# Optimization experiments

Measured on AMD Instinct MI355X. Metric: run time of the kernel, lower is better.

Reference implementation:

```python
import jax, jax.numpy as jnp
import numpy as np


def setup_inputs() -> dict:
    key = jax.random.key(0)
    kq, kk, kv = jax.random.split(key, 3)
    B, HQ, HKV, S, D = 1, 32, 8, 2048, 128
    return {
        "query": jax.random.normal(kq, (B, HQ, S, D), dtype=jnp.float32),
        "key": jax.random.normal(kk, (B, HKV, S, D), dtype=jnp.float32),
        "value": jax.random.normal(kv, (B, HKV, S, D), dtype=jnp.float32),
    }


def reference(query, key, value):
    # RawSDP.forward with is_causal=True, attn_mask=None, dropout_p=0, scale=None
    b, hq, sq, d = query.shape
    hkv = key.shape[1]
    reps = hq // hkv  # GQA group size
    # repeak_kv: expand each kv head `reps` times contiguously along head axis
    key = jnp.repeat(key, reps, axis=1)    # [b, hq, skv, d]
    value = jnp.repeat(value, reps, axis=1)
    skv = key.shape[2]
    half_sqrt = 1.0 / jnp.sqrt(jnp.sqrt(jnp.float32(d)))  # scale split across q and k
    scores = jnp.einsum("bhqd,bhkd->bhqk", query * half_sqrt, key * half_sqrt)
    # causal tril bool mask -> additive mask (0 where allowed, finfo.min where not)
    causal = jnp.tril(jnp.ones((sq, skv), dtype=bool))
    neg = jnp.finfo(query.dtype).min
    scores = scores + jnp.where(causal, jnp.zeros((), query.dtype), neg)
    # softmax computed in float32, cast back to query dtype
    attn = jax.nn.softmax(scores.astype(jnp.float32), axis=-1).astype(query.dtype)
    return jnp.einsum("bhqk,bhkd->bhqd", attn, value)
```

## Files before the change

### kernel.cpp

```cpp
#include <hip/hip_runtime.h>
#include <hip/hip_bf16.h>
#include <stdint.h>

typedef __attribute__((ext_vector_type(8))) short bf16x8;
typedef __attribute__((ext_vector_type(4))) float f32x4;
typedef __attribute__((ext_vector_type(16))) float f32x16;

#define S_LEN 2048
#define D_DIM 128
#define HQ_N  32
#define KVB   32
#define NT    64
#define KTILE_B 8192
#define VTILE_B 8192

__device__ __forceinline__ ushort f2bf(float f) {
  union { float f; uint32_t u; } c; c.f = f;
  uint32_t u = c.u;
  u += 0x7FFFu + ((u >> 16) & 1u);
  return (ushort)(u >> 16);
}

__device__ __forceinline__ uint32_t cvtpk(float lo, float hi) {
  uint32_t r;
  asm("v_cvt_pk_bf16_f32 %0, %1, %2" : "=v"(r) : "v"(lo), "v"(hi));
  return r;
}

__global__ __launch_bounds__(256) void prep_k(const float* __restrict__ K,
                                              ushort* __restrict__ KT) {
  int tid  = blockIdx.x * 256 + threadIdx.x;
  int tile = tid >> 9;
  int c    = tid & 511;
  int s    = c >> 6;
  int lane = c & 63;
  int l31  = lane & 31, hi = lane >> 5;
  const float* src = K + ((size_t)(tile * 32 + l31)) * D_DIM + 16 * s + 8 * hi;
  float4 x = *(const float4*)src;
  float4 y = *(const float4*)(src + 4);
  union { ushort u[8]; bf16x8 v; } o;
  o.u[0] = f2bf(x.x); o.u[1] = f2bf(x.y); o.u[2] = f2bf(x.z); o.u[3] = f2bf(x.w);
  o.u[4] = f2bf(y.x); o.u[5] = f2bf(y.y); o.u[6] = f2bf(y.z); o.u[7] = f2bf(y.w);
  *(bf16x8*)(KT + (size_t)tid * 8) = o.v;
}

__global__ __launch_bounds__(256) void prep_v(const float* __restrict__ V,
                                              ushort* __restrict__ VT) {
  int tid  = blockIdx.x * 256 + threadIdx.x;
  int tile = tid >> 9;
  int cc   = tid & 511;
  int l31  = cc & 31;
  int hi   = (cc >> 5) & 1;
  int c    = (cc >> 6) & 1;
  int dt   = cc >> 7;
  int hkv  = tile >> 6, kt = tile & 63;
  const float* src = V + ((size_t)hkv * S_LEN + kt * 32 + 16 * c + 8 * hi) * D_DIM
                       + 32 * dt + l31;
  union { ushort u[8]; bf16x8 v; } o;
  #pragma unroll
  for (int jj = 0; jj < 8; ++jj) o.u[jj] = f2bf(src[(size_t)jj * D_DIM]);
  *(bf16x8*)(VT + (size_t)tid * 8) = o.v;
}

__global__ __launch_bounds__(64, 2) void attn_fwd(
    const float* __restrict__ Q, const ushort* __restrict__ KT,
    const ushort* __restrict__ VT, float* __restrict__ O) {
  const int id   = blockIdx.x;
  const int g    = id & 7;
  const int rest = id >> 3;
  const int qh   = rest & 3;
  const int j    = 63 - (rest >> 2);
  const int h    = g * 4 + qh;
  const int lane = threadIdx.x;
  const int l31  = lane & 31;
  const int hi   = lane >> 5;
  const int qrow = j * 32 + l31;

  const char* kt_base = (const char*)KT + (size_t)g * NT * KTILE_B;
  const char* vt_base = (const char*)VT + (size_t)g * NT * VTILE_B;

  const float scale = 0.08838834764831845f * 1.4426950408889634f;
  bf16x8 qf[8];
  {
    const float* qp = Q + ((size_t)h * S_LEN + qrow) * D_DIM;
    #pragma unroll
    for (int s = 0; s < 8; ++s) {
      const float* p = qp + 16 * s + 8 * hi;
      float4 x = *(const float4*)p;
      float4 y = *(const float4*)(p + 4);
      bf16x8 f;
      f[0] = (short)f2bf(x.x * scale); f[1] = (short)f2bf(x.y * scale);
      f[2] = (short)f2bf(x.z * scale); f[3] = (short)f2bf(x.w * scale);
      f[4] = (short)f2bf(y.x * scale); f[5] = (short)f2bf(y.y * scale);
      f[6] = (short)f2bf(y.z * scale); f[7] = (short)f2bf(y.w * scale);
      qf[s] = f;
    }
  }

  f32x16 o4[4] = {};
  float mrow = -1e30f, lsum = 0.f;

  for (int kt = 0; kt <= j; ++kt) {
    const char* kp = kt_base + (size_t)kt * KTILE_B;
    const char* vp = vt_base + (size_t)kt * VTILE_B;

    bf16x8 kf[8], vf[8];
    #pragma unroll
    for (int s = 0; s < 8; ++s)
      kf[s] = *(const bf16x8*)(kp + (s * 64 + lane) * 16);
    #pragma unroll
    for (int u = 0; u < 8; ++u)
      vf[u] = *(const bf16x8*)(vp + (u * 64 + lane) * 16);

    f32x16 st = {};
    __builtin_amdgcn_s_setprio(1);
    #pragma unroll
    for (int s = 0; s < 8; ++s)
      st = __builtin_amdgcn_mfma_f32_32x32x16_bf16(kf[s], qf[s], st, 0, 0, 0);
    __builtin_amdgcn_s_setprio(0);

    if (kt == j) {
      #pragma unroll
      for (int r = 0; r < 16; ++r) {
        int kv = KVB * kt + (r & 3) + 8 * (r >> 2) + 4 * hi;
        if (kv > qrow) st[r] = -1e30f;
      }
    }

    float t8[8];
    #pragma unroll
    for (int e = 0; e < 8; ++e) t8[e] = fmaxf(st[e], st[e + 8]);
    float mx = fmaxf(fmaxf(fmaxf(t8[0], t8[1]), fmaxf(t8[2], t8[3])),
                     fmaxf(fmaxf(t8[4], t8[5]), fmaxf(t8[6], t8[7])));
    mx = fmaxf(mx, __shfl_xor(mx, 32));
    float mnew = fmaxf(mrow, mx);
    float alpha = exp2f(mrow - mnew);
    mrow = mnew;

    #pragma unroll
    for (int e = 0; e < 16; ++e) st[e] = exp2f(st[e] - mnew);
    float s8[8];
    #pragma unroll
    for (int e = 0; e < 8; ++e) s8[e] = st[e] + st[e + 8];
    float rsum = ((s8[0] + s8[1]) + (s8[2] + s8[3])) +
                 ((s8[4] + s8[5]) + (s8[6] + s8[7]));
    rsum += __shfl_xor(rsum, 32);
    lsum = lsum * alpha + rsum;

    #pragma unroll
    for (int dt = 0; dt < 4; ++dt) o4[dt] *= alpha;

    bf16x8 pb[2];
    #pragma unroll
    for (int c = 0; c < 2; ++c) {
      const int r0 = c * 8;
      uint32_t a0 = cvtpk(st[r0 + 0], st[r0 + 1]);
      uint32_t b0 = cvtpk(st[r0 + 4], st[r0 + 5]);
      asm volatile("v_permlane32_swap_b32 %0, %1" : "+v"(a0), "+v"(b0));
      uint32_t a1 = cvtpk(st[r0 + 2], st[r0 + 3]);
      uint32_t b1 = cvtpk(st[r0 + 6], st[r0 + 7]);
      asm volatile("v_permlane32_swap_b32 %0, %1" : "+v"(a1), "+v"(b1));
      union { uint32_t u[4]; bf16x8 v; } pu;
      pu.u[0] = a0; pu.u[1] = a1; pu.u[2] = b0; pu.u[3] = b1;
      pb[c] = pu.v;
    }

    __builtin_amdgcn_s_setprio(1);
    #pragma unroll
    for (int dt = 0; dt < 4; ++dt) {
      o4[dt] = __builtin_amdgcn_mfma_f32_32x32x16_bf16(vf[2 * dt + 0], pb[0], o4[dt], 0, 0, 0);
      o4[dt] = __builtin_amdgcn_mfma_f32_32x32x16_bf16(vf[2 * dt + 1], pb[1], o4[dt], 0, 0, 0);
    }
    __builtin_amdgcn_s_setprio(0);
  }

  const float inv = 1.0f / lsum;
  float* op = O + ((size_t)h * S_LEN + qrow) * D_DIM;
  #pragma unroll
  for (int dt = 0; dt < 4; ++dt)
    #pragma unroll
    for (int rq = 0; rq < 4; ++rq) {
      f32x4 vv;
      #pragma unroll
      for (int jj = 0; jj < 4; ++jj) vv[jj] = o4[dt][rq * 4 + jj] * inv;
      *(f32x4*)(op + 32 * dt + 8 * rq + 4 * hi) = vv;
    }
}

extern "C" void kernel_launch(void* const* d_in, const int* in_sizes, int n_in,
                              void* d_out, int out_size, void* d_ws, size_t ws_size,
                              hipStream_t stream) {
  const float* Q = (const float*)d_in[0];
  const float* K = (const float*)d_in[1];
  const float* V = (const float*)d_in[2];
  float* O = (float*)d_out;
  ushort* wsK = (ushort*)d_ws;
  ushort* wsV = wsK + (size_t)8 * NT * (KTILE_B / 2);
  prep_k<<<1024, 256, 0, stream>>>(K, wsK);
  prep_v<<<1024, 256, 0, stream>>>(V, wsV);
  attn_fwd<<<2048, 64, 0, stream>>>(Q, wsK, wsV, O);
}
```

Measured before the change: 83.61 us.

## Double-buffer K tile prefetch and skip rescaling when row max barely grows

Restructures the attention loop into two ping-pong steps so the next K tile is loaded into registers while the current tile's QK MFMAs and softmax run, hiding global load latency. It also adds a lazy rescale: the running max and accumulator rescale happen only when some lane's new max exceeds the old by more than 8 (in log2 units), skipping the alpha multiply on most iterations. The cost is extra VGPRs for the second K buffer, which may pressure the 2-waves-per-SIMD occupancy target. Unscaled exponents can grow up to 2^8 before rescaling, which stays safe in fp32 but slightly changes bf16 rounding of P.

```diff
diff --git a/kernel.cpp b/kernel.cpp
--- a/kernel.cpp
+++ b/kernel.cpp
@@ -62,6 +62,87 @@
   *(bf16x8*)(VT + (size_t)tid * 8) = o.v;
 }
 
+__device__ __forceinline__ void step32(
+    int kt, int j, int qrow, int hi, int lane,
+    const char* kt_base, const char* vt_base,
+    const bf16x8 (&qf)[8], bf16x8 (&KC)[8], bf16x8 (&KN)[8],
+    f32x16 (&o4)[4], float& mrow, float& lsum) {
+  bf16x8 vf[8];
+  const char* vp = vt_base + (size_t)kt * VTILE_B;
+  #pragma unroll
+  for (int u = 0; u < 8; ++u)
+    vf[u] = *(const bf16x8*)(vp + (u * 64 + lane) * 16);
+  if (kt < j) {
+    const char* kp2 = kt_base + (size_t)(kt + 1) * KTILE_B;
+    #pragma unroll
+    for (int s = 0; s < 8; ++s)
+      KN[s] = *(const bf16x8*)(kp2 + (s * 64 + lane) * 16);
+  }
+
+  f32x16 st = {};
+  __builtin_amdgcn_s_setprio(1);
+  #pragma unroll
+  for (int s = 0; s < 8; ++s)
+    st = __builtin_amdgcn_mfma_f32_32x32x16_bf16(KC[s], qf[s], st, 0, 0, 0);
+  __builtin_amdgcn_s_setprio(0);
+
+  if (kt == j) {
+    #pragma unroll
+    for (int r = 0; r < 16; ++r) {
+      int kv = KVB * kt + (r & 3) + 8 * (r >> 2) + 4 * hi;
+      if (kv > qrow) st[r] = -1e30f;
+    }
+  }
+
+  float t8[8];
+  #pragma unroll
+  for (int e = 0; e < 8; ++e) t8[e] = fmaxf(st[e], st[e + 8]);
+  float mx = fmaxf(fmaxf(fmaxf(t8[0], t8[1]), fmaxf(t8[2], t8[3])),
+                   fmaxf(fmaxf(t8[4], t8[5]), fmaxf(t8[6], t8[7])));
+  mx = fmaxf(mx, __shfl_xor(mx, 32));
+  if (!__all(mx <= mrow + 8.0f)) {
+    float mnew = fmaxf(mrow, mx);
+    float alpha = exp2f(mrow - mnew);
+    #pragma unroll
+    for (int dt = 0; dt < 4; ++dt) o4[dt] *= alpha;
+    lsum *= alpha;
+    mrow = mnew;
+  }
+
+  #pragma unroll
+  for (int e = 0; e < 16; ++e) st[e] = exp2f(st[e] - mrow);
+  float s8[8];
+  #pragma unroll
+  for (int e = 0; e < 8; ++e) s8[e] = st[e] + st[e + 8];
+  float rsum = ((s8[0] + s8[1]) + (s8[2] + s8[3])) +
+               ((s8[4] + s8[5]) + (s8[6] + s8[7]));
+  rsum += __shfl_xor(rsum, 32);
+  lsum += rsum;
+
+  bf16x8 pb[2];
+  #pragma unroll
+  for (int c = 0; c < 2; ++c) {
+    const int r0 = c * 8;
+    uint32_t a0 = cvtpk(st[r0 + 0], st[r0 + 1]);
+    uint32_t b0 = cvtpk(st[r0 + 4], st[r0 + 5]);
+    asm volatile("v_permlane32_swap_b32 %0, %1" : "+v"(a0), "+v"(b0));
+    uint32_t a1 = cvtpk(st[r0 + 2], st[r0 + 3]);
+    uint32_t b1 = cvtpk(st[r0 + 6], st[r0 + 7]);
+    asm volatile("v_permlane32_swap_b32 %0, %1" : "+v"(a1), "+v"(b1));
+    union { uint32_t u[4]; bf16x8 v; } pu;
+    pu.u[0] = a0; pu.u[1] = a1; pu.u[2] = b0; pu.u[3] = b1;
+    pb[c] = pu.v;
+  }
+
+  __builtin_amdgcn_s_setprio(1);
+  #pragma unroll
+  for (int dt = 0; dt < 4; ++dt) {
+    o4[dt] = __builtin_amdgcn_mfma_f32_32x32x16_bf16(vf[2 * dt + 0], pb[0], o4[dt], 0, 0, 0);
+    o4[dt] = __builtin_amdgcn_mfma_f32_32x32x16_bf16(vf[2 * dt + 1], pb[1], o4[dt], 0, 0, 0);
+  }
+  __builtin_amdgcn_s_setprio(0);
+}
+
 __global__ __launch_bounds__(64, 2) void attn_fwd(
     const float* __restrict__ Q, const ushort* __restrict__ KT,
     const ushort* __restrict__ VT, float* __restrict__ O) {
@@ -100,78 +181,17 @@
   f32x16 o4[4] = {};
   float mrow = -1e30f, lsum = 0.f;
 
-  for (int kt = 0; kt <= j; ++kt) {
-    const char* kp = kt_base + (size_t)kt * KTILE_B;
-    const char* vp = vt_base + (size_t)kt * VTILE_B;
-
-    bf16x8 kf[8], vf[8];
-    #pragma unroll
-    for (int s = 0; s < 8; ++s)
-      kf[s] = *(const bf16x8*)(kp + (s * 64 + lane) * 16);
-    #pragma unroll
-    for (int u = 0; u < 8; ++u)
-      vf[u] = *(const bf16x8*)(vp + (u * 64 + lane) * 16);
-
-    f32x16 st = {};
-    __builtin_amdgcn_s_setprio(1);
-    #pragma unroll
-    for (int s = 0; s < 8; ++s)
-      st = __builtin_amdgcn_mfma_f32_32x32x16_bf16(kf[s], qf[s], st, 0, 0, 0);
-    __builtin_amdgcn_s_setprio(0);
-
-    if (kt == j) {
-      #pragma unroll
-      for (int r = 0; r < 16; ++r) {
-        int kv = KVB * kt + (r & 3) + 8 * (r >> 2) + 4 * hi;
-        if (kv > qrow) st[r] = -1e30f;
-      }
-    }
-
-    float t8[8];
-    #pragma unroll
-    for (int e = 0; e < 8; ++e) t8[e] = fmaxf(st[e], st[e + 8]);
-    float mx = fmaxf(fmaxf(fmaxf(t8[0], t8[1]), fmaxf(t8[2], t8[3])),
-                     fmaxf(fmaxf(t8[4], t8[5]), fmaxf(t8[6], t8[7])));
-    mx = fmaxf(mx, __shfl_xor(mx, 32));
-    float mnew = fmaxf(mrow, mx);
-    float alpha = exp2f(mrow - mnew);
-    mrow = mnew;
-
-    #pragma unroll
-    for (int e = 0; e < 16; ++e) st[e] = exp2f(st[e] - mnew);
-    float s8[8];
-    #pragma unroll
-    for (int e = 0; e < 8; ++e) s8[e] = st[e] + st[e + 8];
-    float rsum = ((s8[0] + s8[1]) + (s8[2] + s8[3])) +
-                 ((s8[4] + s8[5]) + (s8[6] + s8[7]));
-    rsum += __shfl_xor(rsum, 32);
-    lsum = lsum * alpha + rsum;
-
-    #pragma unroll
-    for (int dt = 0; dt < 4; ++dt) o4[dt] *= alpha;
-
-    bf16x8 pb[2];
-    #pragma unroll
-    for (int c = 0; c < 2; ++c) {
-      const int r0 = c * 8;
-      uint32_t a0 = cvtpk(st[r0 + 0], st[r0 + 1]);
-      uint32_t b0 = cvtpk(st[r0 + 4], st[r0 + 5]);
-      asm volatile("v_permlane32_swap_b32 %0, %1" : "+v"(a0), "+v"(b0));
-      uint32_t a1 = cvtpk(st[r0 + 2], st[r0 + 3]);
-      uint32_t b1 = cvtpk(st[r0 + 6], st[r0 + 7]);
-      asm volatile("v_permlane32_swap_b32 %0, %1" : "+v"(a1), "+v"(b1));
-      union { uint32_t u[4]; bf16x8 v; } pu;
-      pu.u[0] = a0; pu.u[1] = a1; pu.u[2] = b0; pu.u[3] = b1;
-      pb[c] = pu.v;
-    }
-
-    __builtin_amdgcn_s_setprio(1);
-    #pragma unroll
-    for (int dt = 0; dt < 4; ++dt) {
-      o4[dt] = __builtin_amdgcn_mfma_f32_32x32x16_bf16(vf[2 * dt + 0], pb[0], o4[dt], 0, 0, 0);
-      o4[dt] = __builtin_amdgcn_mfma_f32_32x32x16_bf16(vf[2 * dt + 1], pb[1], o4[dt], 0, 0, 0);
-    }
-    __builtin_amdgcn_s_setprio(0);
+  bf16x8 kfa[8], kfb[8];
+  #pragma unroll
+  for (int s = 0; s < 8; ++s)
+    kfa[s] = *(const bf16x8*)(kt_base + (s * 64 + lane) * 16);
+
+  int kt = 0;
+  for (;;) {
+    step32(kt, j, qrow, hi, lane, kt_base, vt_base, qf, kfa, kfb, o4, mrow, lsum);
+    if (++kt > j) break;
+    step32(kt, j, qrow, hi, lane, kt_base, vt_base, qf, kfb, kfa, o4, mrow, lsum);
+    if (++kt > j) break;
   }
 
   const float inv = 1.0f / lsum;
```

After: 82.75 us. No clear change (-1.0%).
